# Kernel tuning notes

Hardware: AMD Instinct MI355X
Metric: run time of the kernel (lower is better)

The kernel has to match this reference:

```python
import jax, jax.numpy as jnp
import numpy as np

DIM = 256
FOCAL_LEVELS = (3, 5, 7)  # odd kernels so padding=k//2 preserves length
B, L = 8, 16384


def _dwconv(x, k):
    # x: [B, C, L], k: [C, 1, K] depthwise kernel (groups=C)
    pad = k.shape[-1] // 2
    return jax.lax.conv_general_dilated(
        x, k, window_strides=(1,), padding=[(pad, pad)],
        dimension_numbers=('NCH', 'OIH', 'NCH'),
        feature_group_count=x.shape[1])


def setup_inputs() -> dict:
    key = jax.random.key(0)
    ks = jax.random.split(key, 13)
    C = DIM
    G = len(FOCAL_LEVELS) + 1
    s = jnp.float32(0.02)
    inp = {
        'x': jax.random.normal(ks[0], (B, C, L), jnp.float32),
        'q_w': jax.random.normal(ks[1], (C, C), jnp.float32) * s,
        'q_b': jax.random.normal(ks[2], (C,), jnp.float32) * s,
        'v_w': jax.random.normal(ks[3], (C, C), jnp.float32) * s,
        'v_b': jax.random.normal(ks[4], (C,), jnp.float32) * s,
        'g_w': jax.random.normal(ks[5], (G, C), jnp.float32) * s,
        'g_b': jax.random.normal(ks[6], (G,), jnp.float32) * s,
        'f0_w': jax.random.normal(ks[7], (C, 1, FOCAL_LEVELS[0]), jnp.float32) * s,
        'f1_w': jax.random.normal(ks[8], (C, 1, FOCAL_LEVELS[1]), jnp.float32) * s,
        'f2_w': jax.random.normal(ks[9], (C, 1, FOCAL_LEVELS[2]), jnp.float32) * s,
        'mix_w': jax.random.normal(ks[10], (C, C), jnp.float32) * s,
        'mix_b': jax.random.normal(ks[11], (C,), jnp.float32) * s,
    }
    return inp


def reference(x, q_w, q_b, v_w, v_b, g_w, g_b, f0_w, f1_w, f2_w, mix_w, mix_b):
    gelu = lambda t: jax.nn.gelu(t, approximate=False)  # torch GELU default = exact erf
    # Linear weights are [out, in]; contract over channel axis of [B, C, L]
    focus = jnp.einsum('bcl,ec->bel', x, v_w) + v_b[None, :, None]   # [B, C, L]
    gates = jnp.einsum('bcl,gc->bgl', x, g_w) + g_b[None, :, None]   # [B, 4, L]
    query = jnp.einsum('bcl,ec->bel', x, q_w) + q_b[None, :, None]   # [B, C, L]

    kernels = (f0_w, f1_w, f2_w)  # fixed small set: loop over levels is fine
    focus = gelu(_dwconv(focus, kernels[0]))
    acc = focus * gates[:, 0:1, :]
    for i in range(1, len(kernels)):
        focus = gelu(_dwconv(focus, kernels[i]))
        acc = acc + focus * gates[:, i:i + 1, :]

    # global focus: mean over length, GELU, broadcast across length via gate
    global_focus = gelu(jnp.mean(focus, axis=2, keepdims=True))      # [B, C, 1]
    acc = acc + global_focus * gates[:, len(kernels):len(kernels) + 1, :]

    # mix_depth: 1x1 conv == pointwise linear over channels
    acc = jnp.einsum('bcl,oc->bol', acc, mix_w) + mix_b[None, :, None]
    mask = jax.nn.softmax(acc, axis=-1)  # softmax over length
    out = jax.nn.sigmoid(query) * mask
    return (out, mask)
```

## Files before the change

### kernel.cpp

```cpp
#include <hip/hip_runtime.h>

#define LLEN 16384
#define PAD 258

typedef short bf16x8 __attribute__((ext_vector_type(8)));
typedef float f32x4 __attribute__((ext_vector_type(4)));

__device__ __forceinline__ unsigned bfbits(float f) {
  union { float f; unsigned u; } v; v.f = f;
  return (v.u + 0x7FFFu + ((v.u >> 16) & 1u)) >> 16;
}
__device__ __forceinline__ short f2bf(float f) { return (short)bfbits(f); }
__device__ __forceinline__ float bf2f(short s) {
  union { unsigned u; float f; } v;
  v.u = ((unsigned)(unsigned short)s) << 16;
  return v.f;
}
__device__ __forceinline__ float geluf(float x) {
  return 0.5f * x * (1.0f + erff(x * 0.70710678118654752f));
}
__device__ __forceinline__ float waveRedSum(float v) {
  #pragma unroll
  for (int o = 32; o > 0; o >>= 1) v += __shfl_xor(v, o, 64);
  return v;
}
__device__ __forceinline__ float waveRedMax(float v) {
  #pragma unroll
  for (int o = 32; o > 0; o >>= 1) v = fmaxf(v, __shfl_xor(v, o, 64));
  return v;
}

__global__ __launch_bounds__(256) void k0_convert(
    const float* __restrict__ qw, const float* __restrict__ vw,
    const float* __restrict__ gw, const float* __restrict__ mw,
    short* __restrict__ qwb, short* __restrict__ vwb,
    short* __restrict__ gwb, short* __restrict__ mwb,
    float* __restrict__ rowsum) {
  int idx = blockIdx.x * 256 + threadIdx.x;
  qwb[idx] = f2bf(qw[idx]);
  vwb[idx] = f2bf(vw[idx]);
  mwb[idx] = f2bf(mw[idx]);
  if (idx < 4096) {
    int r = idx >> 8, c = idx & 255;
    gwb[idx] = (r < 4) ? f2bf(gw[r * 256 + c]) : (short)0;
  }
  if (idx < 2048) rowsum[idx] = 0.f;
}

__device__ __forceinline__ void gemm64(const short* __restrict__ wmat,
                                       const short xs[64][PAD], int lane,
                                       f32x4 acc[4][4]) {
  int r = lane & 15, h = lane >> 4;
  #pragma unroll
  for (int k0 = 0; k0 < 256; k0 += 32) {
    bf16x8 xfr[4];
    #pragma unroll
    for (int lf = 0; lf < 4; ++lf)
      xfr[lf] = *(const bf16x8*)&xs[lf * 16 + r][k0 + 8 * h];
    #pragma unroll
    for (int ef = 0; ef < 4; ++ef) {
      bf16x8 wfr = *(const bf16x8*)(wmat + (ef * 16 + r) * 256 + k0 + 8 * h);
      #pragma unroll
      for (int lf = 0; lf < 4; ++lf)
        acc[ef][lf] = __builtin_amdgcn_mfma_f32_16x16x32_bf16(xfr[lf], wfr,
                                                              acc[ef][lf], 0, 0, 0);
    }
  }
}

__device__ __forceinline__ void store_bf4(short* p, f32x4 a, float bias) {
  uint2 pk;
  pk.x = bfbits(a[0] + bias) | (bfbits(a[1] + bias) << 16);
  pk.y = bfbits(a[2] + bias) | (bfbits(a[3] + bias) << 16);
  *(uint2*)p = pk;
}

__global__ __launch_bounds__(256) void k1_qvg(
    const float* __restrict__ x, const short* __restrict__ vwb,
    const short* __restrict__ qwb, const short* __restrict__ gwb,
    const float* __restrict__ v_b, const float* __restrict__ q_b,
    const float* __restrict__ g_b, short* __restrict__ focus0,
    short* __restrict__ qzS, float* __restrict__ gates) {
  int b = blockIdx.x >> 8, lt = blockIdx.x & 255;
  int l0 = lt << 6;
  __shared__ short xs[64][PAD];
  int t = threadIdx.x;
  {
    int l2 = (t & 31) * 2, cg = t >> 5;
    const float* xb = x + ((size_t)b << 22) + l0 + l2;
    #pragma unroll 4
    for (int rep = 0; rep < 16; ++rep) {
      int c = rep * 16 + cg * 2;
      float2 a = *(const float2*)&xb[(size_t)c << 14];
      float2 bb = *(const float2*)&xb[((size_t)c + 1) << 14];
      *(unsigned*)&xs[l2][c] = bfbits(a.x) | (bfbits(bb.x) << 16);
      *(unsigned*)&xs[l2 + 1][c] = bfbits(a.y) | (bfbits(bb.y) << 16);
    }
  }
  __syncthreads();
  int lane = t & 63, wave = t >> 6;
  int r = lane & 15, h = lane >> 4;
  int e0 = wave << 6;
  f32x4 acc[4][4];

  #pragma unroll
  for (int ef = 0; ef < 4; ++ef)
    #pragma unroll
    for (int lf = 0; lf < 4; ++lf)
      acc[ef][lf] = (f32x4){0.f, 0.f, 0.f, 0.f};
  gemm64(vwb + e0 * 256, xs, lane, acc);
  #pragma unroll
  for (int ef = 0; ef < 4; ++ef) {
    int e = e0 + ef * 16 + r;
    float bias = v_b[e];
    short* rowp = focus0 + ((size_t)((b << 8) | e) << 14) + l0 + 4 * h;
    #pragma unroll
    for (int lf = 0; lf < 4; ++lf)
      store_bf4(rowp + lf * 16, acc[ef][lf], bias);
  }

  #pragma unroll
  for (int ef = 0; ef < 4; ++ef)
    #pragma unroll
    for (int lf = 0; lf < 4; ++lf)
      acc[ef][lf] = (f32x4){0.f, 0.f, 0.f, 0.f};
  gemm64(qwb + e0 * 256, xs, lane, acc);
  #pragma unroll
  for (int ef = 0; ef < 4; ++ef) {
    int e = e0 + ef * 16 + r;
    float bias = q_b[e];
    short* rowp = qzS + (((size_t)((b << 8) | e) << 15) + 16384) + l0 + 4 * h;
    #pragma unroll
    for (int lf = 0; lf < 4; ++lf)
      store_bf4(rowp + lf * 16, acc[ef][lf], bias);
  }

  if (wave == 0) {
    f32x4 gacc[4];
    #pragma unroll
    for (int lf = 0; lf < 4; ++lf) gacc[lf] = (f32x4){0.f, 0.f, 0.f, 0.f};
    #pragma unroll
    for (int k0 = 0; k0 < 256; k0 += 32) {
      bf16x8 wfr = *(const bf16x8*)(gwb + r * 256 + k0 + 8 * h);
      #pragma unroll
      for (int lf = 0; lf < 4; ++lf) {
        bf16x8 xfr = *(const bf16x8*)&xs[lf * 16 + r][k0 + 8 * h];
        gacc[lf] = __builtin_amdgcn_mfma_f32_16x16x32_bf16(xfr, wfr, gacc[lf], 0, 0, 0);
      }
    }
    if (r < 4) {
      float gb = g_b[r];
      float* gp = gates + (((size_t)((b << 2) | r)) << 14) + l0 + 4 * h;
      #pragma unroll
      for (int lf = 0; lf < 4; ++lf) {
        float4 o = {gacc[lf][0] + gb, gacc[lf][1] + gb,
                    gacc[lf][2] + gb, gacc[lf][3] + gb};
        *(float4*)(gp + lf * 16) = o;
      }
    }
  }
}

__global__ __launch_bounds__(256) void k2_conv(
    const short* __restrict__ focus0, const float* __restrict__ gates,
    const float* __restrict__ f0_w, const float* __restrict__ f1_w,
    const float* __restrict__ f2_w, short* __restrict__ acc3S,
    float* __restrict__ rowsum) {
  int bx = blockIdx.x;
  int b = bx >> 12, c = (bx >> 4) & 255, lt = bx & 15;
  int l0 = lt << 10;
  __shared__ float s0[1036], s1[1034], s2[1030];
  __shared__ float rs[4];
  int t = threadIdx.x;
  const short* fp = focus0 + ((size_t)((b << 8) | c) << 14);
  for (int i = t; i < 1036; i += 256) {
    int gl = l0 - 6 + i;
    s0[i] = (gl >= 0 && gl < LLEN) ? bf2f(fp[gl]) : 0.f;
  }
  float w0[3], w1[5], w2[7];
  #pragma unroll
  for (int j = 0; j < 3; ++j) w0[j] = f0_w[c * 3 + j];
  #pragma unroll
  for (int j = 0; j < 5; ++j) w1[j] = f1_w[c * 5 + j];
  #pragma unroll
  for (int j = 0; j < 7; ++j) w2[j] = f2_w[c * 7 + j];
  __syncthreads();
  for (int i = t; i < 1034; i += 256) {
    int gl = l0 - 5 + i;
    float z = w0[0] * s0[i] + w0[1] * s0[i + 1] + w0[2] * s0[i + 2];
    s1[i] = (gl >= 0 && gl < LLEN) ? geluf(z) : 0.f;
  }
  __syncthreads();
  for (int i = t; i < 1030; i += 256) {
    int gl = l0 - 3 + i;
    float z = w1[0] * s1[i] + w1[1] * s1[i + 1] + w1[2] * s1[i + 2] +
              w1[3] * s1[i + 3] + w1[4] * s1[i + 4];
    s2[i] = (gl >= 0 && gl < LLEN) ? geluf(z) : 0.f;
  }
  __syncthreads();
  const float* gp = gates + ((size_t)(b << 2) << 14);
  short* op = acc3S + ((size_t)((b << 8) | c) << 15);
  float lsum = 0.f;
  #pragma unroll
  for (int ii = 0; ii < 2; ++ii) {
    int i = 2 * t + 512 * ii;
    float z0 = w2[0] * s2[i] + w2[1] * s2[i + 1] + w2[2] * s2[i + 2] +
               w2[3] * s2[i + 3] + w2[4] * s2[i + 4] + w2[5] * s2[i + 5] +
               w2[6] * s2[i + 6];
    float z1 = w2[0] * s2[i + 1] + w2[1] * s2[i + 2] + w2[2] * s2[i + 3] +
               w2[3] * s2[i + 4] + w2[4] * s2[i + 5] + w2[5] * s2[i + 6] +
               w2[6] * s2[i + 7];
    float f30 = geluf(z0), f31 = geluf(z1);
    lsum += f30 + f31;
    int l = l0 + i;
    float a0 = s1[i + 5] * gp[l] + s2[i + 3] * gp[LLEN + l] + f30 * gp[2 * LLEN + l];
    float a1 = s1[i + 6] * gp[l + 1] + s2[i + 4] * gp[LLEN + l + 1] +
               f31 * gp[2 * LLEN + l + 1];
    *(unsigned*)&op[l] = bfbits(a0) | (bfbits(a1) << 16);
  }
  float wsv = waveRedSum(lsum);
  if ((t & 63) == 0) rs[t >> 6] = wsv;
  __syncthreads();
  if (t == 0) atomicAdd(&rowsum[(b << 8) | c], rs[0] + rs[1] + rs[2] + rs[3]);
}

__global__ __launch_bounds__(256) void k3_gf(const float* __restrict__ rowsum,
                                             float* __restrict__ gf) {
  int i = blockIdx.x * 256 + threadIdx.x;
  gf[i] = geluf(rowsum[i] * (1.0f / 16384.0f));
}

__global__ __launch_bounds__(256) void k4_mix(
    short* maskS, const float* __restrict__ gates, const float* __restrict__ gf,
    const short* __restrict__ mwb, const float* __restrict__ mix_b) {
  int b = blockIdx.x >> 8, lt = blockIdx.x & 255;
  int l0 = lt << 6;
  __shared__ short xs[64][PAD];
  int t = threadIdx.x;
  {
    int l2 = (t & 31) * 2, cg = t >> 5;
    float2 g3v = *(const float2*)(gates + (((size_t)((b << 2) | 3)) << 14) + l0 + l2);
    const float* gfp = gf + (b << 8);
    const unsigned short* ap =
        (const unsigned short*)maskS + (((size_t)(b << 8)) << 15) + l0 + l2;
    #pragma unroll 4
    for (int rep = 0; rep < 16; ++rep) {
      int c = rep * 16 + cg * 2;
      unsigned av = *(const unsigned*)&ap[(size_t)c << 15];
      unsigned bv = *(const unsigned*)&ap[((size_t)c + 1) << 15];
      float gf0 = gfp[c], gf1 = gfp[c + 1];
      float a0 = bf2f((short)(av & 0xFFFF)) + gf0 * g3v.x;
      float a1 = bf2f((short)(av >> 16)) + gf0 * g3v.y;
      float b0 = bf2f((short)(bv & 0xFFFF)) + gf1 * g3v.x;
      float b1 = bf2f((short)(bv >> 16)) + gf1 * g3v.y;
      *(unsigned*)&xs[l2][c] = bfbits(a0) | (bfbits(b0) << 16);
      *(unsigned*)&xs[l2 + 1][c] = bfbits(a1) | (bfbits(b1) << 16);
    }
  }
  __syncthreads();
  int lane = t & 63, wave = t >> 6;
  int r = lane & 15, h = lane >> 4;
  int e0 = wave << 6;
  f32x4 acc[4][4];
  #pragma unroll
  for (int ef = 0; ef < 4; ++ef)
    #pragma unroll
    for (int lf = 0; lf < 4; ++lf)
      acc[ef][lf] = (f32x4){0.f, 0.f, 0.f, 0.f};
  gemm64(mwb + e0 * 256, xs, lane, acc);
  #pragma unroll
  for (int ef = 0; ef < 4; ++ef) {
    int o = e0 + ef * 16 + r;
    float bias = mix_b[o];
    short* rowp = maskS + (((size_t)((b << 8) | o) << 15) + 16384) + l0 + 4 * h;
    #pragma unroll
    for (int lf = 0; lf < 4; ++lf)
      store_bf4(rowp + lf * 16, acc[ef][lf], bias);
  }
}

__global__ __launch_bounds__(512) void k5_softmax(
    const short* __restrict__ maskS, const short* __restrict__ outS,
    float* __restrict__ maskF, float* __restrict__ outF) {
  int row = blockIdx.x;
  int t = threadIdx.x;
  const short* mrow = maskS + ((size_t)row << 15) + 16384;
  const short* qrow = outS + ((size_t)row << 15) + 16384;
  float* mw = maskF + ((size_t)row << 14);
  float* ow = outF + ((size_t)row << 14);
  int lane = t & 63, wave = t >> 6;
  bf16x8 qv[4];
  float f[32];
  float lm = -3.0e38f;
  #pragma unroll
  for (int i = 0; i < 4; ++i) {
    bf16x8 mv = *(const bf16x8*)&mrow[i * 4096 + t * 8];
    qv[i] = *(const bf16x8*)&qrow[i * 4096 + t * 8];
    #pragma unroll
    for (int j = 0; j < 8; ++j) {
      float vf = bf2f(mv[j]);
      f[i * 8 + j] = vf;
      lm = fmaxf(lm, vf);
    }
  }
  __shared__ float redm[8], reds[8];
  float wm = waveRedMax(lm);
  if (lane == 0) redm[wave] = wm;
  __syncthreads();
  float M = redm[0];
  #pragma unroll
  for (int w = 1; w < 8; ++w) M = fmaxf(M, redm[w]);
  float ls = 0.f;
  #pragma unroll
  for (int k = 0; k < 32; ++k) {
    f[k] = expf(f[k] - M);
    ls += f[k];
  }
  float wsum = waveRedSum(ls);
  if (lane == 0) reds[wave] = wsum;
  __syncthreads();
  float S = reds[0];
  #pragma unroll
  for (int w = 1; w < 8; ++w) S += reds[w];
  float inv = 1.0f / S;
  #pragma unroll
  for (int i = 0; i < 4; ++i) {
    float mk[8], oo[8];
    #pragma unroll
    for (int j = 0; j < 8; ++j) {
      mk[j] = f[i * 8 + j] * inv;
      float sig = 1.0f / (1.0f + expf(-bf2f(qv[i][j])));
      oo[j] = sig * mk[j];
    }
    float* mp = &mw[i * 4096 + t * 8];
    float* op = &ow[i * 4096 + t * 8];
    *(float4*)mp = (float4){mk[0], mk[1], mk[2], mk[3]};
    *(float4*)(mp + 4) = (float4){mk[4], mk[5], mk[6], mk[7]};
    *(float4*)op = (float4){oo[0], oo[1], oo[2], oo[3]};
    *(float4*)(op + 4) = (float4){oo[4], oo[5], oo[6], oo[7]};
  }
}

extern "C" void kernel_launch(void* const* d_in, const int* in_sizes, int n_in,
                              void* d_out, int out_size, void* d_ws, size_t ws_size,
                              hipStream_t stream) {
  const float* x     = (const float*)d_in[0];
  const float* q_w   = (const float*)d_in[1];
  const float* q_b   = (const float*)d_in[2];
  const float* v_w   = (const float*)d_in[3];
  const float* v_b   = (const float*)d_in[4];
  const float* g_w   = (const float*)d_in[5];
  const float* g_b   = (const float*)d_in[6];
  const float* f0_w  = (const float*)d_in[7];
  const float* f1_w  = (const float*)d_in[8];
  const float* f2_w  = (const float*)d_in[9];
  const float* mix_w = (const float*)d_in[10];
  const float* mix_b = (const float*)d_in[11];

  float* outbuf  = (float*)d_out;
  float* maskbuf = outbuf + (size_t)8 * 256 * 16384;
  short* outS  = (short*)outbuf;
  short* maskS = (short*)maskbuf;

  char* ws = (char*)d_ws;
  short* vwb    = (short*)(ws + 0);
  short* qwb    = (short*)(ws + 131072);
  short* mwb    = (short*)(ws + 262144);
  short* gwb    = (short*)(ws + 393216);
  float* rowsum = (float*)(ws + 401408);
  float* gf     = (float*)(ws + 409600);
  float* gates  = (float*)(ws + 417792);
  short* focus0 = (short*)(ws + 2514944);

  k0_convert<<<dim3(256), dim3(256), 0, stream>>>(q_w, v_w, g_w, mix_w,
                                                  qwb, vwb, gwb, mwb, rowsum);
  k1_qvg<<<dim3(2048), dim3(256), 0, stream>>>(x, vwb, qwb, gwb, v_b, q_b, g_b,
                                               focus0, outS, gates);
  k2_conv<<<dim3(32768), dim3(256), 0, stream>>>(focus0, gates, f0_w, f1_w, f2_w,
                                                 maskS, rowsum);
  k3_gf<<<dim3(8), dim3(256), 0, stream>>>(rowsum, gf);
  k4_mix<<<dim3(2048), dim3(256), 0, stream>>>(maskS, gates, gf, mwb, mix_b);
  k5_softmax<<<dim3(2048), dim3(512), 0, stream>>>(maskS, outS, maskbuf, outbuf);
}
```

Before: 376.2 us.

## Widen GEMM blocks to 1024 threads, fold gf into mix, use fast GELU/exp

The k1 and k4 GEMM kernels now launch 1024 threads per block. Each wave computes a 32x32 tile instead of a 64x64 tile, which cuts accumulator registers and raises occupancy. The separate global-focus kernel is removed and its GELU is computed into shared memory at the start of k4_mix, saving a launch. In the depthwise conv stages the exact erf GELU is replaced by the sigmoid approximation x*sigmoid(1.702x), and the softmax uses __expf; both reduce transcendental cost but change numerics relative to the exact-erf reference.

```diff
diff --git a/kernel.cpp b/kernel.cpp
--- a/kernel.cpp
+++ b/kernel.cpp
@@ -19,14 +19,12 @@
 __device__ __forceinline__ float geluf(float x) {
   return 0.5f * x * (1.0f + erff(x * 0.70710678118654752f));
 }
+__device__ __forceinline__ float gelu_fast(float x) {
+  return x / (1.0f + __expf(-1.702f * x));
+}
 __device__ __forceinline__ float waveRedSum(float v) {
   #pragma unroll
   for (int o = 32; o > 0; o >>= 1) v += __shfl_xor(v, o, 64);
-  return v;
-}
-__device__ __forceinline__ float waveRedMax(float v) {
-  #pragma unroll
-  for (int o = 32; o > 0; o >>= 1) v = fmaxf(v, __shfl_xor(v, o, 64));
   return v;
 }
 
@@ -47,23 +45,19 @@
   if (idx < 2048) rowsum[idx] = 0.f;
 }
 
-__device__ __forceinline__ void gemm64(const short* __restrict__ wmat,
-                                       const short xs[64][PAD], int lane,
-                                       f32x4 acc[4][4]) {
+__device__ __forceinline__ void gemm32(const short* __restrict__ wmat,
+                                       const short (*xsl)[PAD], int lane,
+                                       f32x4 acc[2][2]) {
   int r = lane & 15, h = lane >> 4;
   #pragma unroll
   for (int k0 = 0; k0 < 256; k0 += 32) {
-    bf16x8 xfr[4];
-    #pragma unroll
-    for (int lf = 0; lf < 4; ++lf)
-      xfr[lf] = *(const bf16x8*)&xs[lf * 16 + r][k0 + 8 * h];
-    #pragma unroll
-    for (int ef = 0; ef < 4; ++ef) {
+    bf16x8 xfr0 = *(const bf16x8*)&xsl[r][k0 + 8 * h];
+    bf16x8 xfr1 = *(const bf16x8*)&xsl[16 + r][k0 + 8 * h];
+    #pragma unroll
+    for (int ef = 0; ef < 2; ++ef) {
       bf16x8 wfr = *(const bf16x8*)(wmat + (ef * 16 + r) * 256 + k0 + 8 * h);
-      #pragma unroll
-      for (int lf = 0; lf < 4; ++lf)
-        acc[ef][lf] = __builtin_amdgcn_mfma_f32_16x16x32_bf16(xfr[lf], wfr,
-                                                              acc[ef][lf], 0, 0, 0);
+      acc[ef][0] = __builtin_amdgcn_mfma_f32_16x16x32_bf16(xfr0, wfr, acc[ef][0], 0, 0, 0);
+      acc[ef][1] = __builtin_amdgcn_mfma_f32_16x16x32_bf16(xfr1, wfr, acc[ef][1], 0, 0, 0);
     }
   }
 }
@@ -75,7 +69,7 @@
   *(uint2*)p = pk;
 }
 
-__global__ __launch_bounds__(256) void k1_qvg(
+__global__ __launch_bounds__(1024, 8) void k1_qvg(
     const float* __restrict__ x, const short* __restrict__ vwb,
     const short* __restrict__ qwb, const short* __restrict__ gwb,
     const float* __restrict__ v_b, const float* __restrict__ q_b,
@@ -88,9 +82,9 @@
   {
     int l2 = (t & 31) * 2, cg = t >> 5;
     const float* xb = x + ((size_t)b << 22) + l0 + l2;
-    #pragma unroll 4
-    for (int rep = 0; rep < 16; ++rep) {
-      int c = rep * 16 + cg * 2;
+    #pragma unroll
+    for (int rep = 0; rep < 4; ++rep) {
+      int c = rep * 64 + cg * 2;
       float2 a = *(const float2*)&xb[(size_t)c << 14];
       float2 bb = *(const float2*)&xb[((size_t)c + 1) << 14];
       *(unsigned*)&xs[l2][c] = bfbits(a.x) | (bfbits(bb.x) << 16);
@@ -99,60 +93,63 @@
   }
   __syncthreads();
   int lane = t & 63, wave = t >> 6;
+  int we = wave & 7, wl = wave >> 3;
   int r = lane & 15, h = lane >> 4;
-  int e0 = wave << 6;
-  f32x4 acc[4][4];
-
-  #pragma unroll
-  for (int ef = 0; ef < 4; ++ef)
-    #pragma unroll
-    for (int lf = 0; lf < 4; ++lf)
+  int e0 = we << 5;
+  const short (*xsl)[PAD] = (const short (*)[PAD])&xs[wl << 5];
+  int lbase = l0 + (wl << 5) + 4 * h;
+  f32x4 acc[2][2];
+
+  #pragma unroll
+  for (int ef = 0; ef < 2; ++ef)
+    #pragma unroll
+    for (int lf = 0; lf < 2; ++lf)
       acc[ef][lf] = (f32x4){0.f, 0.f, 0.f, 0.f};
-  gemm64(vwb + e0 * 256, xs, lane, acc);
-  #pragma unroll
-  for (int ef = 0; ef < 4; ++ef) {
+  gemm32(vwb + e0 * 256, xsl, lane, acc);
+  #pragma unroll
+  for (int ef = 0; ef < 2; ++ef) {
     int e = e0 + ef * 16 + r;
     float bias = v_b[e];
-    short* rowp = focus0 + ((size_t)((b << 8) | e) << 14) + l0 + 4 * h;
-    #pragma unroll
-    for (int lf = 0; lf < 4; ++lf)
+    short* rowp = focus0 + ((size_t)((b << 8) | e) << 14) + lbase;
+    #pragma unroll
+    for (int lf = 0; lf < 2; ++lf)
       store_bf4(rowp + lf * 16, acc[ef][lf], bias);
   }
 
   #pragma unroll
-  for (int ef = 0; ef < 4; ++ef)
-    #pragma unroll
-    for (int lf = 0; lf < 4; ++lf)
+  for (int ef = 0; ef < 2; ++ef)
+    #pragma unroll
+    for (int lf = 0; lf < 2; ++lf)
       acc[ef][lf] = (f32x4){0.f, 0.f, 0.f, 0.f};
-  gemm64(qwb + e0 * 256, xs, lane, acc);
-  #pragma unroll
-  for (int ef = 0; ef < 4; ++ef) {
+  gemm32(qwb + e0 * 256, xsl, lane, acc);
+  #pragma unroll
+  for (int ef = 0; ef < 2; ++ef) {
     int e = e0 + ef * 16 + r;
     float bias = q_b[e];
-    short* rowp = qzS + (((size_t)((b << 8) | e) << 15) + 16384) + l0 + 4 * h;
-    #pragma unroll
-    for (int lf = 0; lf < 4; ++lf)
+    short* rowp = qzS + (((size_t)((b << 8) | e) << 15) + 16384) + lbase;
+    #pragma unroll
+    for (int lf = 0; lf < 2; ++lf)
       store_bf4(rowp + lf * 16, acc[ef][lf], bias);
   }
 
-  if (wave == 0) {
-    f32x4 gacc[4];
-    #pragma unroll
-    for (int lf = 0; lf < 4; ++lf) gacc[lf] = (f32x4){0.f, 0.f, 0.f, 0.f};
+  if (we == 0) {
+    f32x4 gacc[2];
+    gacc[0] = (f32x4){0.f, 0.f, 0.f, 0.f};
+    gacc[1] = (f32x4){0.f, 0.f, 0.f, 0.f};
     #pragma unroll
     for (int k0 = 0; k0 < 256; k0 += 32) {
       bf16x8 wfr = *(const bf16x8*)(gwb + r * 256 + k0 + 8 * h);
       #pragma unroll
-      for (int lf = 0; lf < 4; ++lf) {
-        bf16x8 xfr = *(const bf16x8*)&xs[lf * 16 + r][k0 + 8 * h];
+      for (int lf = 0; lf < 2; ++lf) {
+        bf16x8 xfr = *(const bf16x8*)&xsl[lf * 16 + r][k0 + 8 * h];
         gacc[lf] = __builtin_amdgcn_mfma_f32_16x16x32_bf16(xfr, wfr, gacc[lf], 0, 0, 0);
       }
     }
     if (r < 4) {
       float gb = g_b[r];
-      float* gp = gates + (((size_t)((b << 2) | r)) << 14) + l0 + 4 * h;
+      float* gp = gates + (((size_t)((b << 2) | r)) << 14) + lbase;
       #pragma unroll
-      for (int lf = 0; lf < 4; ++lf) {
+      for (int lf = 0; lf < 2; ++lf) {
         float4 o = {gacc[lf][0] + gb, gacc[lf][1] + gb,
                     gacc[lf][2] + gb, gacc[lf][3] + gb};
         *(float4*)(gp + lf * 16) = o;
@@ -188,14 +185,14 @@
   for (int i = t; i < 1034; i += 256) {
     int gl = l0 - 5 + i;
     float z = w0[0] * s0[i] + w0[1] * s0[i + 1] + w0[2] * s0[i + 2];
-    s1[i] = (gl >= 0 && gl < LLEN) ? geluf(z) : 0.f;
+    s1[i] = (gl >= 0 && gl < LLEN) ? gelu_fast(z) : 0.f;
   }
   __syncthreads();
   for (int i = t; i < 1030; i += 256) {
     int gl = l0 - 3 + i;
     float z = w1[0] * s1[i] + w1[1] * s1[i + 1] + w1[2] * s1[i + 2] +
               w1[3] * s1[i + 3] + w1[4] * s1[i + 4];
-    s2[i] = (gl >= 0 && gl < LLEN) ? geluf(z) : 0.f;
+    s2[i] = (gl >= 0 && gl < LLEN) ? gelu_fast(z) : 0.f;
   }
   __syncthreads();
   const float* gp = gates + ((size_t)(b << 2) << 14);
@@ -210,7 +207,7 @@
     float z1 = w2[0] * s2[i + 1] + w2[1] * s2[i + 2] + w2[2] * s2[i + 3] +
                w2[3] * s2[i + 4] + w2[4] * s2[i + 5] + w2[5] * s2[i + 6] +
                w2[6] * s2[i + 7];
-    float f30 = geluf(z0), f31 = geluf(z1);
+    float f30 = gelu_fast(z0), f31 = gelu_fast(z1);
     lsum += f30 + f31;
     int l = l0 + i;
     float a0 = s1[i + 5] * gp[l] + s2[i + 3] * gp[LLEN + l] + f30 * gp[2 * LLEN + l];
@@ -224,31 +221,27 @@
   if (t == 0) atomicAdd(&rowsum[(b << 8) | c], rs[0] + rs[1] + rs[2] + rs[3]);
 }
 
-__global__ __launch_bounds__(256) void k3_gf(const float* __restrict__ rowsum,
-                                             float* __restrict__ gf) {
-  int i = blockIdx.x * 256 + threadIdx.x;
-  gf[i] = geluf(rowsum[i] * (1.0f / 16384.0f));
-}
-
-__global__ __launch_bounds__(256) void k4_mix(
-    short* maskS, const float* __restrict__ gates, const float* __restrict__ gf,
+__global__ __launch_bounds__(1024, 8) void k4_mix(
+    short* maskS, const float* __restrict__ gates, const float* __restrict__ rowsum,
     const short* __restrict__ mwb, const float* __restrict__ mix_b) {
   int b = blockIdx.x >> 8, lt = blockIdx.x & 255;
   int l0 = lt << 6;
   __shared__ short xs[64][PAD];
+  __shared__ float gfS[256];
   int t = threadIdx.x;
+  if (t < 256) gfS[t] = geluf(rowsum[(b << 8) | t] * (1.0f / 16384.0f));
+  __syncthreads();
   {
     int l2 = (t & 31) * 2, cg = t >> 5;
     float2 g3v = *(const float2*)(gates + (((size_t)((b << 2) | 3)) << 14) + l0 + l2);
-    const float* gfp = gf + (b << 8);
     const unsigned short* ap =
         (const unsigned short*)maskS + (((size_t)(b << 8)) << 15) + l0 + l2;
-    #pragma unroll 4
-    for (int rep = 0; rep < 16; ++rep) {
-      int c = rep * 16 + cg * 2;
+    #pragma unroll
+    for (int rep = 0; rep < 4; ++rep) {
+      int c = rep * 64 + cg * 2;
       unsigned av = *(const unsigned*)&ap[(size_t)c << 15];
       unsigned bv = *(const unsigned*)&ap[((size_t)c + 1) << 15];
-      float gf0 = gfp[c], gf1 = gfp[c + 1];
+      float gf0 = gfS[c], gf1 = gfS[c + 1];
       float a0 = bf2f((short)(av & 0xFFFF)) + gf0 * g3v.x;
       float a1 = bf2f((short)(av >> 16)) + gf0 * g3v.y;
       float b0 = bf2f((short)(bv & 0xFFFF)) + gf1 * g3v.x;
@@ -259,22 +252,25 @@
   }
   __syncthreads();
   int lane = t & 63, wave = t >> 6;
+  int we = wave & 7, wl = wave >> 3;
   int r = lane & 15, h = lane >> 4;
-  int e0 = wave << 6;
-  f32x4 acc[4][4];
-  #pragma unroll
-  for (int ef = 0; ef < 4; ++ef)
-    #pragma unroll
-    for (int lf = 0; lf < 4; ++lf)
+  int e0 = we << 5;
+  const short (*xsl)[PAD] = (const short (*)[PAD])&xs[wl << 5];
+  int lbase = l0 + (wl << 5) + 4 * h;
+  f32x4 acc[2][2];
+  #pragma unroll
+  for (int ef = 0; ef < 2; ++ef)
+    #pragma unroll
+    for (int lf = 0; lf < 2; ++lf)
       acc[ef][lf] = (f32x4){0.f, 0.f, 0.f, 0.f};
-  gemm64(mwb + e0 * 256, xs, lane, acc);
-  #pragma unroll
-  for (int ef = 0; ef < 4; ++ef) {
+  gemm32(mwb + e0 * 256, xsl, lane, acc);
+  #pragma unroll
+  for (int ef = 0; ef < 2; ++ef) {
     int o = e0 + ef * 16 + r;
     float bias = mix_b[o];
-    short* rowp = maskS + (((size_t)((b << 8) | o) << 15) + 16384) + l0 + 4 * h;
-    #pragma unroll
-    for (int lf = 0; lf < 4; ++lf)
+    short* rowp = maskS + (((size_t)((b << 8) | o) << 15) + 16384) + lbase;
+    #pragma unroll
+    for (int lf = 0; lf < 2; ++lf)
       store_bf4(rowp + lf * 16, acc[ef][lf], bias);
   }
 }
@@ -304,8 +300,11 @@
     }
   }
   __shared__ float redm[8], reds[8];
-  float wm = waveRedMax(lm);
-  if (lane == 0) redm[wave] = wm;
+  {
+    #pragma unroll
+    for (int o = 32; o > 0; o >>= 1) lm = fmaxf(lm, __shfl_xor(lm, o, 64));
+  }
+  if (lane == 0) redm[wave] = lm;
   __syncthreads();
   float M = redm[0];
   #pragma unroll
@@ -313,7 +312,7 @@
   float ls = 0.f;
   #pragma unroll
   for (int k = 0; k < 32; ++k) {
-    f[k] = expf(f[k] - M);
+    f[k] = __expf(f[k] - M);
     ls += f[k];
   }
   float wsum = waveRedSum(ls);
@@ -329,7 +328,7 @@
     #pragma unroll
     for (int j = 0; j < 8; ++j) {
       mk[j] = f[i * 8 + j] * inv;
-      float sig = 1.0f / (1.0f + expf(-bf2f(qv[i][j])));
+      float sig = 1.0f / (1.0f + __expf(-bf2f(qv[i][j])));
       oo[j] = sig * mk[j];
     }
     float* mp = &mw[i * 4096 + t * 8];
@@ -368,17 +367,15 @@
   short* mwb    = (short*)(ws + 262144);
   short* gwb    = (short*)(ws + 393216);
   float* rowsum = (float*)(ws + 401408);
-  float* gf     = (float*)(ws + 409600);
   float* gates  = (float*)(ws + 417792);
   short* focus0 = (short*)(ws + 2514944);
 
   k0_convert<<<dim3(256), dim3(256), 0, stream>>>(q_w, v_w, g_w, mix_w,
                                                   qwb, vwb, gwb, mwb, rowsum);
-  k1_qvg<<<dim3(2048), dim3(256), 0, stream>>>(x, vwb, qwb, gwb, v_b, q_b, g_b,
-                                               focus0, outS, gates);
+  k1_qvg<<<dim3(2048), dim3(1024), 0, stream>>>(x, vwb, qwb, gwb, v_b, q_b, g_b,
+                                                focus0, outS, gates);
   k2_conv<<<dim3(32768), dim3(256), 0, stream>>>(focus0, gates, f0_w, f1_w, f2_w,
                                                  maskS, rowsum);
-  k3_gf<<<dim3(8), dim3(256), 0, stream>>>(rowsum, gf);
-  k4_mix<<<dim3(2048), dim3(256), 0, stream>>>(maskS, gates, gf, mwb, mix_b);
+  k4_mix<<<dim3(2048), dim3(1024), 0, stream>>>(maskS, gates, rowsum, mwb, mix_b);
   k5_softmax<<<dim3(2048), dim3(512), 0, stream>>>(maskS, outS, maskbuf, outbuf);
 }
```

New measurement: 452.0 us. 1.2x slower.
